# Kernel tuning notes

Hardware: AMD Instinct MI355X
Metric: run time of the kernel (lower is better)

Reference implementation:

```python
import jax, jax.numpy as jnp
import numpy as np

EPS_COV = 0.01  # module eps added to covariance diagonal
G, N_MEM = 8, 64  # groups, channels per group


def _pade_coeffs(m=5):
    # Taylor coefficients of sqrt(1 - x): c_k = (-1)^k * binom(1/2, k)
    c = np.zeros(2 * m + 1)
    c[0] = 1.0
    b = 1.0
    for k in range(1, 2 * m + 1):
        b *= (0.5 - (k - 1)) / k
        c[k] = ((-1) ** k) * b
    # Pade [m/m]: q_0 = 1, solve sum_j q_j c_{k-j} = 0 for k = m+1..2m
    A = np.zeros((m, m))
    rhs = np.zeros(m)
    for i in range(m):
        k = m + 1 + i
        for j in range(m):
            A[i, j] = c[k - (j + 1)]
        rhs[i] = -c[k]
    q = np.concatenate([[1.0], np.linalg.solve(A, rhs)])
    p = np.array([sum(q[j] * c[k - j] for j in range(min(k, m) + 1)) for k in range(m + 1)])
    return p, q

_PADE_P, _PADE_Q = _pade_coeffs(5)


def matrix_pade_approximant(p, I):
    # evaluates the [5/5] Pade approximant of sqrt at p (normalized SPD matrix)
    pp = jnp.asarray(_PADE_P, dtype=p.dtype)
    pq = jnp.asarray(_PADE_Q, dtype=p.dtype)
    p_app = I - p
    p_sqrt = pp[0] * I
    q_sqrt = pq[0] * I
    p_hat = p_app
    for i in range(5):
        p_sqrt = p_sqrt + pp[i + 1] * p_hat
        q_sqrt = q_sqrt + pq[i + 1] * p_hat
        p_hat = p_hat @ p_app
    return jnp.linalg.solve(q_sqrt, p_sqrt)


def mpa_sqrt(M):
    # batched matrix square root via Pade approximant (MPA_Lya.forward)
    normM = jnp.linalg.norm(M, axis=(1, 2))[:, None, None]
    n = M.shape[1]
    I = jnp.broadcast_to(jnp.eye(n, dtype=M.dtype), M.shape)
    return matrix_pade_approximant(M / normM, I) * jnp.sqrt(normM)


def setup_inputs() -> dict:
    key = jax.random.key(0)
    k1, k2 = jax.random.split(key)
    x = jax.random.normal(k1, (32, 512, 64, 64), dtype=jnp.float32)
    weight = jax.random.uniform(k2, (G, N_MEM, 1), dtype=jnp.float32)
    bias = jnp.zeros((G, N_MEM, 1), dtype=jnp.float32)
    return {"x": x, "weight": weight, "bias": bias}


def reference(x, weight, bias):
    N, C, H, W = x.shape
    n_mem = C // G
    xg = jnp.transpose(x, (1, 0, 2, 3)).reshape(G, n_mem, -1)  # (G, n_mem, N*H*W)
    mu = jnp.mean(xg, axis=2, keepdims=True)
    xg = xg - mu
    I = jnp.eye(n_mem, dtype=x.dtype)[None]
    xxt = jnp.einsum('gim,gjm->gij', xg, xg) / (N * H * W) + I * EPS_COV
    subspace = jnp.linalg.inv(mpa_sqrt(xxt))  # ZCA whitening matrix per group
    xr = jnp.einsum('gij,gjm->gim', subspace, xg)
    xr = xr * weight + bias
    xr = xr.reshape(C, N, H, W)
    return jnp.transpose(xr, (1, 0, 2, 3))
```

## Files before the change

kernel.cpp:

```cpp
#include <hip/hip_runtime.h>

#define NBATCH 32
#define CHAN   512
#define HWSZ   4096
#define NG     8
#define NM     64
#define MTOT   (NBATCH * HWSZ)
#define EPSC   0.01f
#define P68    68

typedef _Float16 f16;
typedef _Float16 f16x8 __attribute__((ext_vector_type(8)));
typedef float    f32x4 __attribute__((ext_vector_type(4)));

#define MFMA16(a, b, c) __builtin_amdgcn_mfma_f32_16x16x32_f16(a, b, c, 0, 0, 0)

__global__ __launch_bounds__(256) void gram_k(const float* __restrict__ x,
                                              float* __restrict__ gpart,
                                              float* __restrict__ spart) {
    __shared__ __align__(16) f16 tile[64 * 128];
    __shared__ float red[2][4096];

    const int bid  = blockIdx.x;
    const int g    = bid >> 6;
    const int n    = (bid >> 1) & 31;
    const int half = bid & 1;
    const float* xb = x + ((size_t)(n * CHAN + g * NM)) * HWSZ + half * 2048;

    const int t = threadIdx.x;
    const int w = t >> 6;
    const int l = t & 63;

    f32x4 acc[4][4];
#pragma unroll
    for (int i = 0; i < 4; ++i)
#pragma unroll
        for (int j = 0; j < 4; ++j) acc[i][j] = (f32x4){0.f, 0.f, 0.f, 0.f};
    float fsum[4] = {0.f, 0.f, 0.f, 0.f};

    for (int tt = 0; tt < 16; ++tt) {
        const float* xt = xb + tt * 128;
#pragma unroll
        for (int i = 0; i < 4; ++i) {
            const int p    = t + 256 * i;
            const int ch   = p >> 4;
            const int off8 = (p & 15) * 8;
            const float4 v0 = *(const float4*)(xt + (size_t)ch * HWSZ + off8);
            const float4 v1 = *(const float4*)(xt + (size_t)ch * HWSZ + off8 + 4);
            fsum[i] += (v0.x + v0.y) + (v0.z + v0.w) + (v1.x + v1.y) + (v1.z + v1.w);
            f16x8 hv;
            hv[0] = (f16)v0.x; hv[1] = (f16)v0.y; hv[2] = (f16)v0.z; hv[3] = (f16)v0.w;
            hv[4] = (f16)v1.x; hv[5] = (f16)v1.y; hv[6] = (f16)v1.z; hv[7] = (f16)v1.w;
            *(f16x8*)&tile[ch * 128 + (off8 ^ ((ch & 7) << 3))] = hv;
        }
        __syncthreads();

        f16x8 frag[4];
#pragma unroll
        for (int rb = 0; rb < 4; ++rb) {
            const int ch = rb * 16 + (l & 15);
            const int k0 = w * 32 + (l >> 4) * 8;
            frag[rb] = *(const f16x8*)&tile[ch * 128 + (k0 ^ ((ch & 7) << 3))];
        }
#pragma unroll
        for (int i = 0; i < 4; ++i)
#pragma unroll
            for (int j = 0; j < 4; ++j)
                acc[i][j] = MFMA16(frag[i], frag[j], acc[i][j]);
        __syncthreads();
    }

#pragma unroll
    for (int i = 0; i < 4; ++i) {
        fsum[i] += __shfl_xor(fsum[i], 1);
        fsum[i] += __shfl_xor(fsum[i], 2);
        fsum[i] += __shfl_xor(fsum[i], 4);
        fsum[i] += __shfl_xor(fsum[i], 8);
    }
    if ((l & 15) == 0) {
        const int chb = t >> 4;
#pragma unroll
        for (int i = 0; i < 4; ++i)
            spart[(size_t)bid * 64 + chb + 16 * i] = fsum[i];
    }

    if (w >= 2) {
#pragma unroll
        for (int i = 0; i < 4; ++i)
#pragma unroll
            for (int j = 0; j < 4; ++j)
#pragma unroll
                for (int r = 0; r < 4; ++r) {
                    const int row = i * 16 + (l >> 4) * 4 + r;
                    const int col = j * 16 + (l & 15);
                    red[w - 2][row * 64 + col] = acc[i][j][r];
                }
    }
    __syncthreads();
    if (w < 2) {
#pragma unroll
        for (int i = 0; i < 4; ++i)
#pragma unroll
            for (int j = 0; j < 4; ++j)
#pragma unroll
                for (int r = 0; r < 4; ++r) {
                    const int row = i * 16 + (l >> 4) * 4 + r;
                    const int col = j * 16 + (l & 15);
                    red[w][row * 64 + col] += acc[i][j][r];
                }
    }
    __syncthreads();
#pragma unroll
    for (int k = 0; k < 16; ++k) {
        const int e = t + 256 * k;
        gpart[(size_t)bid * 4096 + e] = red[0][e] + red[1][e];
    }
}

__global__ __launch_bounds__(256) void solve_k(const float* __restrict__ gpart,
                                               const float* __restrict__ spart,
                                               const float* __restrict__ wgt,
                                               const float* __restrict__ bias,
                                               f16* __restrict__ Tf,
                                               float* __restrict__ offv) {
    __shared__ __align__(16) float A[64 * P68];
    __shared__ __align__(16) float B[64 * P68];
    __shared__ __align__(16) float Cc[64 * P68];
    __shared__ __align__(16) float Dd[64 * P68];
    __shared__ float mus[64];
    __shared__ float red[4];
    __shared__ float tr16[16];

    const int g = blockIdx.x, t = threadIdx.x;

    float covv[16], cov2[16];
#pragma unroll
    for (int k = 0; k < 16; ++k) { covv[k] = 0.f; cov2[k] = 0.f; }
    for (int p = 0; p < 64; p += 2) {
        const float* gp0 = gpart + ((size_t)(g * 64 + p)) * 4096;
        const float* gp1 = gp0 + 4096;
#pragma unroll
        for (int k = 0; k < 16; ++k) {
            covv[k] += gp0[t + 256 * k];
            cov2[k] += gp1[t + 256 * k];
        }
    }
#pragma unroll
    for (int k = 0; k < 16; ++k) covv[k] += cov2[k];

    if (t < 64) {
        float ss = 0.f;
#pragma unroll 8
        for (int p = 0; p < 64; ++p) ss += spart[(size_t)(g * 64 + p) * 64 + t];
        mus[t] = ss * (1.0f / MTOT);
    }
    __syncthreads();

    float loc = 0.f;
#pragma unroll
    for (int k = 0; k < 16; ++k) {
        const int e = t + 256 * k;
        const int i = e >> 6, j = e & 63;
        const float cv = covv[k] * (1.0f / MTOT) - mus[i] * mus[j] + (i == j ? EPSC : 0.f);
        covv[k] = cv;
        loc += cv * cv;
    }
#pragma unroll
    for (int o = 32; o > 0; o >>= 1) loc += __shfl_down(loc, o);
    if ((t & 63) == 0) red[t >> 6] = loc;
    __syncthreads();
    const float normM = sqrtf(red[0] + red[1] + red[2] + red[3]);
    const float ninv  = 1.0f / normM;

#pragma unroll
    for (int k = 0; k < 16; ++k) {
        const int e = t + 256 * k;
        const int i = e >> 6, j = e & 63;
        const float pa = (i == j ? 1.f : 0.f) - covv[k] * ninv;
        A[i * P68 + j] = pa;
        B[i * P68 + j] = pa;
    }
    __syncthreads();

    const int ty = t >> 4, tx = t & 15;
    const int i0 = ty * 4, j0 = tx * 4;

    const float PP[6] = {1.f, -2.75f, 2.75f, -1.203125f, 0.21484375f, -0.0107421875f};
    const float QQ[6] = {1.f, -2.25f, 1.75f, -0.546875f, 0.05859375f, -0.0009765625f};

    float pacc[4][4], qacc[4][4];
#pragma unroll
    for (int ai = 0; ai < 4; ++ai)
#pragma unroll
        for (int bi = 0; bi < 4; ++bi) {
            const int i = i0 + ai, j = j0 + bi;
            const float pa = A[i * P68 + j];
            const float id = (i == j) ? 1.f : 0.f;
            pacc[ai][bi] = PP[0] * id + PP[1] * pa;
            qacc[ai][bi] = QQ[0] * id + QQ[1] * pa;
        }

    float* src = B;
    float* dst = Cc;
    for (int s = 0; s < 4; ++s) {
        float mm[4][4];
#pragma unroll
        for (int ai = 0; ai < 4; ++ai)
#pragma unroll
            for (int bi = 0; bi < 4; ++bi) mm[ai][bi] = 0.f;
        for (int kk = 0; kk < 64; ++kk) {
            const float4 a4 = *(const float4*)&src[kk * P68 + i0];
            const float4 b4 = *(const float4*)&A[kk * P68 + j0];
            const float av[4] = {a4.x, a4.y, a4.z, a4.w};
            const float bv[4] = {b4.x, b4.y, b4.z, b4.w};
#pragma unroll
            for (int ai = 0; ai < 4; ++ai)
#pragma unroll
                for (int bi = 0; bi < 4; ++bi)
                    mm[ai][bi] = fmaf(av[ai], bv[bi], mm[ai][bi]);
        }
#pragma unroll
        for (int ai = 0; ai < 4; ++ai) {
            float4 w4;
            w4.x = mm[ai][0]; w4.y = mm[ai][1]; w4.z = mm[ai][2]; w4.w = mm[ai][3];
            *(float4*)&dst[(i0 + ai) * P68 + j0] = w4;
        }
#pragma unroll
        for (int ai = 0; ai < 4; ++ai)
#pragma unroll
            for (int bi = 0; bi < 4; ++bi) {
                pacc[ai][bi] = fmaf(PP[s + 2], mm[ai][bi], pacc[ai][bi]);
                qacc[ai][bi] = fmaf(QQ[s + 2], mm[ai][bi], qacc[ai][bi]);
            }
        __syncthreads();
        float* tmpp = src; src = dst; dst = tmpp;
    }

    if (ty == tx)
        tr16[tx] = pacc[0][0] + pacc[1][1] + pacc[2][2] + pacc[3][3];
    __syncthreads();
    float trsum = 0.f;
#pragma unroll
    for (int i = 0; i < 16; ++i) trsum += tr16[i];
    const float cP   = trsum * (1.0f / 64.0f);
    const float icP  = 1.0f / cP;

#pragma unroll
    for (int ai = 0; ai < 4; ++ai) {
        float4 we, wq;
        const int i = i0 + ai;
        we.x = pacc[ai][0] * icP - (i == j0 + 0 ? 1.f : 0.f);
        we.y = pacc[ai][1] * icP - (i == j0 + 1 ? 1.f : 0.f);
        we.z = pacc[ai][2] * icP - (i == j0 + 2 ? 1.f : 0.f);
        we.w = pacc[ai][3] * icP - (i == j0 + 3 ? 1.f : 0.f);
        wq.x = qacc[ai][0]; wq.y = qacc[ai][1]; wq.z = qacc[ai][2]; wq.w = qacc[ai][3];
        *(float4*)&A[i * P68 + j0] = we;
        *(float4*)&B[i * P68 + j0] = wq;
    }
    __syncthreads();

    float* rsrc = B;
    float* rdst = Cc;
    for (int it = 0; it < 6; ++it) {
        float mm[4][4];
#pragma unroll
        for (int ai = 0; ai < 4; ++ai)
#pragma unroll
            for (int bi = 0; bi < 4; ++bi) mm[ai][bi] = 0.f;
        for (int kk = 0; kk < 64; ++kk) {
            const float4 a4 = *(const float4*)&A[kk * P68 + i0];
            const float4 b4 = *(const float4*)&rsrc[kk * P68 + j0];
            const float av[4] = {a4.x, a4.y, a4.z, a4.w};
            const float bv[4] = {b4.x, b4.y, b4.z, b4.w};
#pragma unroll
            for (int ai = 0; ai < 4; ++ai)
#pragma unroll
                for (int bi = 0; bi < 4; ++bi)
                    mm[ai][bi] = fmaf(av[ai], bv[bi], mm[ai][bi]);
        }
#pragma unroll
        for (int ai = 0; ai < 4; ++ai) {
            const float4 q4 = *(const float4*)&B[(i0 + ai) * P68 + j0];
            float4 w4;
            w4.x = q4.x - mm[ai][0]; w4.y = q4.y - mm[ai][1];
            w4.z = q4.z - mm[ai][2]; w4.w = q4.w - mm[ai][3];
            *(float4*)&rdst[(i0 + ai) * P68 + j0] = w4;
        }
        __syncthreads();
        if (it == 0) { rsrc = Cc; rdst = Dd; }
        else { float* tmpp = rsrc; rsrc = rdst; rdst = tmpp; }
    }
    float* X = rsrc;

    const float invs = icP / sqrtf(normM);
    if (t < 64) {
        float sm = 0.f;
        for (int j = 0; j < 64; ++j) sm += X[t * P68 + j] * mus[j];
        offv[g * NM + t] = bias[g * NM + t] - sm * invs * wgt[g * NM + t];
    }
#pragma unroll
    for (int k = 0; k < 16; ++k) {
        const int e = t + 256 * k;
        const int i = e >> 6, j = e & 63;
        Tf[(size_t)g * 4096 + e] = (f16)(X[i * P68 + j] * invs * wgt[g * NM + i]);
    }
}

__global__ __launch_bounds__(256) void apply_k(const float* __restrict__ x,
                                               const f16* __restrict__ Tf,
                                               const float* __restrict__ offv,
                                               float* __restrict__ out) {
    __shared__ __align__(16) f16 xs[128 * 64];
    __shared__ __align__(16) f16 Ts[4096];
    __shared__ float offs[64];

    const int bid  = blockIdx.x;
    const int g    = bid >> 6;
    const int n    = (bid >> 1) & 31;
    const int half = bid & 1;
    const size_t base = ((size_t)(n * CHAN + g * NM)) * HWSZ + half * 2048;
    const float* xb = x + base;
    float* ob = out + base;

    const int t = threadIdx.x;
    const int w = t >> 6;
    const int l = t & 63;

#pragma unroll
    for (int i = 0; i < 2; ++i) {
        const int c   = t + 256 * i;
        const int oc  = c >> 3;
        const int icb = (c & 7) * 8;
        const f16x8 v = *(const f16x8*)&Tf[(size_t)g * 4096 + oc * 64 + icb];
        *(f16x8*)&Ts[oc * 64 + (icb ^ ((oc & 7) << 3))] = v;
    }
    if (t < 64) offs[t] = offv[g * NM + t];
    __syncthreads();

    f16x8 afrag[2];
#pragma unroll
    for (int c = 0; c < 2; ++c) {
        const int oc = w * 16 + (l & 15);
        const int k0 = c * 32 + (l >> 4) * 8;
        afrag[c] = *(const f16x8*)&Ts[oc * 64 + (k0 ^ ((oc & 7) << 3))];
    }
    float offr[4];
#pragma unroll
    for (int r = 0; r < 4; ++r) offr[r] = offs[w * 16 + (l >> 4) * 4 + r];

    for (int tt = 0; tt < 16; ++tt) {
        const float* xt = xb + tt * 128;
        __syncthreads();
#pragma unroll
        for (int i = 0; i < 4; ++i) {
            const int p    = t + 256 * i;
            const int ch   = p >> 4;
            const int off8 = (p & 15) * 8;
            const float4 v0 = *(const float4*)(xt + (size_t)ch * HWSZ + off8);
            const float4 v1 = *(const float4*)(xt + (size_t)ch * HWSZ + off8 + 4);
            f16 h[8];
            h[0] = (f16)v0.x; h[1] = (f16)v0.y; h[2] = (f16)v0.z; h[3] = (f16)v0.w;
            h[4] = (f16)v1.x; h[5] = (f16)v1.y; h[6] = (f16)v1.z; h[7] = (f16)v1.w;
#pragma unroll
            for (int j = 0; j < 8; ++j) {
                const int pos = off8 + j;
                xs[pos * 64 + (ch ^ (((pos ^ (pos >> 3)) & 7) << 3))] = h[j];
            }
        }
        __syncthreads();

#pragma unroll
        for (int pb = 0; pb < 8; ++pb) {
            f32x4 acc;
            acc[0] = offr[0]; acc[1] = offr[1]; acc[2] = offr[2]; acc[3] = offr[3];
            const int pos = pb * 16 + (l & 15);
            const int swz = ((pos ^ (pos >> 3)) & 7) << 3;
#pragma unroll
            for (int c = 0; c < 2; ++c) {
                const int k0 = c * 32 + (l >> 4) * 8;
                const f16x8 bfrag = *(const f16x8*)&xs[pos * 64 + (k0 ^ swz)];
                acc = MFMA16(afrag[c], bfrag, acc);
            }
            const int posg = tt * 128 + pb * 16 + (l & 15);
#pragma unroll
            for (int r = 0; r < 4; ++r) {
                const int oc = w * 16 + (l >> 4) * 4 + r;
                ob[(size_t)oc * HWSZ + posg] = acc[r];
            }
        }
    }
}

extern "C" void kernel_launch(void* const* d_in, const int* in_sizes, int n_in,
                              void* d_out, int out_size, void* d_ws, size_t ws_size,
                              hipStream_t stream) {
    const float* x    = (const float*)d_in[0];
    const float* wgt  = (const float*)d_in[1];
    const float* bias = (const float*)d_in[2];
    float* out = (float*)d_out;

    float* ws    = (float*)d_ws;
    float* gpart = ws;
    float* spart = ws + 2097152;
    float* offv  = ws + 2129920;
    f16*   Tf    = (f16*)(ws + 2130432);

    gram_k <<<512, 256, 0, stream>>>(x, gpart, spart);
    solve_k<<<8,   256, 0, stream>>>(gpart, spart, wgt, bias, Tf, offv);
    apply_k<<<512, 256, 0, stream>>>(x, Tf, offv, out);
}
```

Before: 239.8 us.

## Emit fp16 fragment-ordered copy of x in gram pass for apply kernel

The gram kernel now also transposes each tile in LDS and writes an fp16 copy of x to workspace, laid out in MFMA B-fragment order. The apply kernel reads this half-width copy directly into registers, with no LDS staging, no barriers and no fp32-to-fp16 conversion, and loads the transform and offsets straight from global memory. The aim is to halve the bytes apply reads and remove its shuffle work. The cost is an extra global write and a byte-granular LDS scatter in the gram kernel, and the second read of x can no longer be served from cache.

```diff
diff --git a/kernel.cpp b/kernel.cpp
--- a/kernel.cpp
+++ b/kernel.cpp
@@ -17,9 +17,12 @@
 
 __global__ __launch_bounds__(256) void gram_k(const float* __restrict__ x,
                                               float* __restrict__ gpart,
-                                              float* __restrict__ spart) {
-    __shared__ __align__(16) f16 tile[64 * 128];
-    __shared__ float red[2][4096];
+                                              float* __restrict__ spart,
+                                              f16* __restrict__ xh) {
+    __shared__ __align__(16) char smem[32768];
+    f16* tileA = (f16*)smem;
+    f16* tileB = (f16*)(smem + 16384);
+    float* red = (float*)smem;
 
     const int bid  = blockIdx.x;
     const int g    = bid >> 6;
@@ -48,10 +51,18 @@
             const float4 v0 = *(const float4*)(xt + (size_t)ch * HWSZ + off8);
             const float4 v1 = *(const float4*)(xt + (size_t)ch * HWSZ + off8 + 4);
             fsum[i] += (v0.x + v0.y) + (v0.z + v0.w) + (v1.x + v1.y) + (v1.z + v1.w);
+            f16 h[8];
+            h[0] = (f16)v0.x; h[1] = (f16)v0.y; h[2] = (f16)v0.z; h[3] = (f16)v0.w;
+            h[4] = (f16)v1.x; h[5] = (f16)v1.y; h[6] = (f16)v1.z; h[7] = (f16)v1.w;
             f16x8 hv;
-            hv[0] = (f16)v0.x; hv[1] = (f16)v0.y; hv[2] = (f16)v0.z; hv[3] = (f16)v0.w;
-            hv[4] = (f16)v1.x; hv[5] = (f16)v1.y; hv[6] = (f16)v1.z; hv[7] = (f16)v1.w;
-            *(f16x8*)&tile[ch * 128 + (off8 ^ ((ch & 7) << 3))] = hv;
+#pragma unroll
+            for (int j = 0; j < 8; ++j) hv[j] = h[j];
+            *(f16x8*)&tileA[ch * 128 + (off8 ^ ((ch & 7) << 3))] = hv;
+#pragma unroll
+            for (int j = 0; j < 8; ++j) {
+                const int pos = off8 + j;
+                tileB[pos * 64 + (ch ^ (((pos ^ (pos >> 3)) & 7) << 3))] = h[j];
+            }
         }
         __syncthreads();
 
@@ -60,13 +71,25 @@
         for (int rb = 0; rb < 4; ++rb) {
             const int ch = rb * 16 + (l & 15);
             const int k0 = w * 32 + (l >> 4) * 8;
-            frag[rb] = *(const f16x8*)&tile[ch * 128 + (k0 ^ ((ch & 7) << 3))];
+            frag[rb] = *(const f16x8*)&tileA[ch * 128 + (k0 ^ ((ch & 7) << 3))];
         }
 #pragma unroll
         for (int i = 0; i < 4; ++i)
 #pragma unroll
             for (int j = 0; j < 4; ++j)
                 acc[i][j] = MFMA16(frag[i], frag[j], acc[i][j]);
+
+#pragma unroll
+        for (int i = 0; i < 4; ++i) {
+            const int q   = t + 256 * i;
+            const int pb  = (q >> 6) & 7;
+            const int ql  = q & 63;
+            const int pos = pb * 16 + (ql & 15);
+            const int k0  = (q >> 9) * 32 + (ql >> 4) * 8;
+            const int swz = ((pos ^ (pos >> 3)) & 7) << 3;
+            const f16x8 v = *(const f16x8*)&tileB[pos * 64 + (k0 ^ swz)];
+            *(f16x8*)&xh[((size_t)(bid * 16 + tt) * 1024 + q) * 8] = v;
+        }
         __syncthreads();
     }
 
@@ -93,7 +116,7 @@
                 for (int r = 0; r < 4; ++r) {
                     const int row = i * 16 + (l >> 4) * 4 + r;
                     const int col = j * 16 + (l & 15);
-                    red[w - 2][row * 64 + col] = acc[i][j][r];
+                    red[(w - 2) * 4096 + row * 64 + col] = acc[i][j][r];
                 }
     }
     __syncthreads();
@@ -106,14 +129,14 @@
                 for (int r = 0; r < 4; ++r) {
                     const int row = i * 16 + (l >> 4) * 4 + r;
                     const int col = j * 16 + (l & 15);
-                    red[w][row * 64 + col] += acc[i][j][r];
+                    red[w * 4096 + row * 64 + col] += acc[i][j][r];
                 }
     }
     __syncthreads();
 #pragma unroll
     for (int k = 0; k < 16; ++k) {
         const int e = t + 256 * k;
-        gpart[(size_t)bid * 4096 + e] = red[0][e] + red[1][e];
+        gpart[(size_t)bid * 4096 + e] = red[e] + red[4096 + e];
     }
 }
 
@@ -242,8 +265,8 @@
     float trsum = 0.f;
 #pragma unroll
     for (int i = 0; i < 16; ++i) trsum += tr16[i];
-    const float cP   = trsum * (1.0f / 64.0f);
-    const float icP  = 1.0f / cP;
+    const float cP  = trsum * (1.0f / 64.0f);
+    const float icP = 1.0f / cP;
 
 #pragma unroll
     for (int ai = 0; ai < 4; ++ai) {
@@ -306,79 +329,41 @@
     }
 }
 
-__global__ __launch_bounds__(256) void apply_k(const float* __restrict__ x,
+__global__ __launch_bounds__(256) void apply_k(const f16* __restrict__ xh,
                                                const f16* __restrict__ Tf,
                                                const float* __restrict__ offv,
                                                float* __restrict__ out) {
-    __shared__ __align__(16) f16 xs[128 * 64];
-    __shared__ __align__(16) f16 Ts[4096];
-    __shared__ float offs[64];
-
     const int bid  = blockIdx.x;
     const int g    = bid >> 6;
     const int n    = (bid >> 1) & 31;
     const int half = bid & 1;
-    const size_t base = ((size_t)(n * CHAN + g * NM)) * HWSZ + half * 2048;
-    const float* xb = x + base;
-    float* ob = out + base;
+    float* ob = out + ((size_t)(n * CHAN + g * NM)) * HWSZ + half * 2048;
 
     const int t = threadIdx.x;
     const int w = t >> 6;
     const int l = t & 63;
 
-#pragma unroll
-    for (int i = 0; i < 2; ++i) {
-        const int c   = t + 256 * i;
-        const int oc  = c >> 3;
-        const int icb = (c & 7) * 8;
-        const f16x8 v = *(const f16x8*)&Tf[(size_t)g * 4096 + oc * 64 + icb];
-        *(f16x8*)&Ts[oc * 64 + (icb ^ ((oc & 7) << 3))] = v;
-    }
-    if (t < 64) offs[t] = offv[g * NM + t];
-    __syncthreads();
-
     f16x8 afrag[2];
 #pragma unroll
     for (int c = 0; c < 2; ++c) {
         const int oc = w * 16 + (l & 15);
-        const int k0 = c * 32 + (l >> 4) * 8;
-        afrag[c] = *(const f16x8*)&Ts[oc * 64 + (k0 ^ ((oc & 7) << 3))];
+        afrag[c] = *(const f16x8*)&Tf[(size_t)g * 4096 + oc * 64 + c * 32 + (l >> 4) * 8];
     }
     float offr[4];
 #pragma unroll
-    for (int r = 0; r < 4; ++r) offr[r] = offs[w * 16 + (l >> 4) * 4 + r];
+    for (int r = 0; r < 4; ++r) offr[r] = offv[g * NM + w * 16 + (l >> 4) * 4 + r];
+
+    const f16* xt = xh + (size_t)bid * 131072;
 
     for (int tt = 0; tt < 16; ++tt) {
-        const float* xt = xb + tt * 128;
-        __syncthreads();
-#pragma unroll
-        for (int i = 0; i < 4; ++i) {
-            const int p    = t + 256 * i;
-            const int ch   = p >> 4;
-            const int off8 = (p & 15) * 8;
-            const float4 v0 = *(const float4*)(xt + (size_t)ch * HWSZ + off8);
-            const float4 v1 = *(const float4*)(xt + (size_t)ch * HWSZ + off8 + 4);
-            f16 h[8];
-            h[0] = (f16)v0.x; h[1] = (f16)v0.y; h[2] = (f16)v0.z; h[3] = (f16)v0.w;
-            h[4] = (f16)v1.x; h[5] = (f16)v1.y; h[6] = (f16)v1.z; h[7] = (f16)v1.w;
-#pragma unroll
-            for (int j = 0; j < 8; ++j) {
-                const int pos = off8 + j;
-                xs[pos * 64 + (ch ^ (((pos ^ (pos >> 3)) & 7) << 3))] = h[j];
-            }
-        }
-        __syncthreads();
-
+        const f16* xtt = xt + tt * 8192;
 #pragma unroll
         for (int pb = 0; pb < 8; ++pb) {
             f32x4 acc;
             acc[0] = offr[0]; acc[1] = offr[1]; acc[2] = offr[2]; acc[3] = offr[3];
-            const int pos = pb * 16 + (l & 15);
-            const int swz = ((pos ^ (pos >> 3)) & 7) << 3;
 #pragma unroll
             for (int c = 0; c < 2; ++c) {
-                const int k0 = c * 32 + (l >> 4) * 8;
-                const f16x8 bfrag = *(const f16x8*)&xs[pos * 64 + (k0 ^ swz)];
+                const f16x8 bfrag = *(const f16x8*)&xtt[((c * 8 + pb) * 64 + l) * 8];
                 acc = MFMA16(afrag[c], bfrag, acc);
             }
             const int posg = tt * 128 + pb * 16 + (l & 15);
@@ -404,8 +389,9 @@
     float* spart = ws + 2097152;
     float* offv  = ws + 2129920;
     f16*   Tf    = (f16*)(ws + 2130432);
-
-    gram_k <<<512, 256, 0, stream>>>(x, gpart, spart);
+    f16*   xh    = (f16*)(ws + 2146816);
+
+    gram_k <<<512, 256, 0, stream>>>(x, gpart, spart, xh);
     solve_k<<<8,   256, 0, stream>>>(gpart, spart, wgt, bias, Tf, offv);
-    apply_k<<<512, 256, 0, stream>>>(x, Tf, offv, out);
+    apply_k<<<512, 256, 0, stream>>>(xh, Tf, offv, out);
 }
```

New measurement: 292.7 us. 1.22x slower.
